# Performance work log

Hardware: AMD Instinct MI355X
Metric: run time of the kernel (lower is better)

The kernel has to match this reference:

```python
import jax, jax.numpy as jnp
import numpy as np

BATCH, EMBED, HIDDEN, VOCAB = 128, 512, 512, 32000
MAX_SEQ_LEN = 20  # self.max_seq_length in the torch module; static for jit


def setup_inputs() -> dict:
    key = jax.random.key(0)
    ks = jax.random.split(key, 9)
    w = lambda k, shape: (jax.random.normal(k, shape, jnp.float32) * 0.05)
    return {
        "features": jax.random.normal(ks[0], (BATCH, EMBED), jnp.float32),
        "lengths": jnp.full((BATCH,), MAX_SEQ_LEN, dtype=jnp.int32),
        "emb_table": w(ks[1], (VOCAB, EMBED)),
        # nn.LSTM (single layer) params, PyTorch gate order i,f,g,o
        "W_ih": w(ks[2], (4 * HIDDEN, EMBED)),
        "W_hh": w(ks[3], (4 * HIDDEN, HIDDEN)),
        "b_ih": w(ks[4], (4 * HIDDEN,)),
        "b_hh": w(ks[5], (4 * HIDDEN,)),
        # fc_out
        "W_fc": w(ks[6], (VOCAB, HIDDEN)),
        "b_fc": w(ks[7], (VOCAB,)),
    }


def reference(features, lengths, emb_table, W_ih, W_hh, b_ih, b_hh, W_fc, b_fc):
    B = features.shape[0]
    H = W_hh.shape[1]
    h0 = jnp.zeros((B, H), features.dtype)
    c0 = jnp.zeros((B, H), features.dtype)
    bias = b_ih + b_hh

    def step(carry, _):
        h, c, x = carry  # x: [B, E] current input token embedding
        gates = x @ W_ih.T + h @ W_hh.T + bias          # [B, 4H]
        i_g, f_g, g_g, o_g = jnp.split(gates, 4, axis=-1)
        c = jax.nn.sigmoid(f_g) * c + jax.nn.sigmoid(i_g) * jnp.tanh(g_g)
        h = jax.nn.sigmoid(o_g) * jnp.tanh(c)
        logits = h @ W_fc.T + b_fc                      # [B, V]
        idx = jnp.argmax(logits, axis=-1)               # greedy token
        val = jnp.max(logits, axis=-1)
        return (h, c, emb_table[idx]), (idx, val)

    _, (ids, vals) = jax.lax.scan(step, (h0, c0, features), None, length=MAX_SEQ_LEN)
    # [T, B] -> [B, T] to match torch.stack(..., 1)
    return jnp.transpose(ids), jnp.transpose(vals)
```

## Files before the change

kernel.cpp:

```cpp
#include <hip/hip_runtime.h>
#include <hip/hip_bf16.h>
#include <math.h>


#define B 128
#define E 512
#define H 512
#define V 32000
#define TSEQ 20
#define NG 2048
#define KSPLIT 16
#define NBLK_L 250
#define PKPAD 256

typedef __attribute__((ext_vector_type(8))) short short8v;
typedef __attribute__((ext_vector_type(4))) float f32x4;
typedef unsigned long long ull;

__device__ __forceinline__ float sigmoidf_(float x) { return 1.0f / (1.0f + expf(-x)); }

__device__ __forceinline__ short f2bf_s(float x) {
    __hip_bfloat16 h = __float2bfloat16(x);
    return *reinterpret_cast<short*>(&h);
}
__device__ __forceinline__ float bfs2f(short s) {
    __hip_bfloat16 h = *reinterpret_cast<__hip_bfloat16*>(&s);
    return __bfloat162float(h);
}
__device__ __forceinline__ ull shflx_u64(ull x, int m) {
    int lo = __shfl_xor((int)(unsigned int)x, m);
    int hi = __shfl_xor((int)(unsigned int)(x >> 32), m);
    return ((ull)(unsigned int)hi << 32) | (unsigned int)lo;
}
__device__ __forceinline__ void merge2(ull& k1, ull& k2, ull o1, ull o2) {
    ull a = k1 > o1 ? k1 : o1;
    ull b = k1 > o1 ? o1 : k1;
    ull c = k2 > o2 ? k2 : o2;
    k1 = a;
    k2 = b > c ? b : c;
}
__device__ __forceinline__ ull makekey(float v, unsigned int n) {
    unsigned int u = __float_as_uint(v);
    u ^= (unsigned int)(((int)u >> 31)) | 0x80000000u;
    return ((ull)u << 32) | (0xFFFFFFFFu - n);
}
__device__ __forceinline__ int keyidx(ull k) {
    return (int)(0xFFFFFFFFu - (unsigned int)(k & 0xFFFFFFFFu));
}

__global__ __launch_bounds__(256) void wsplit_pack_kernel(const float* __restrict__ W,
                                                          short* __restrict__ Wph,
                                                          short* __restrict__ Wpl) {
    size_t gid = (size_t)blockIdx.x * 256 + threadIdx.x;
    size_t i = gid * 8;
    int n = (int)(i >> 9);
    int k0 = (int)(i & 511);
    float4 a = *reinterpret_cast<const float4*>(W + i);
    float4 b = *reinterpret_cast<const float4*>(W + i + 4);
    float xv[8] = {a.x, a.y, a.z, a.w, b.x, b.y, b.z, b.w};
    union { short8v v; short s[8]; } uh, ul;
#pragma unroll
    for (int j = 0; j < 8; ++j) {
        short hs = f2bf_s(xv[j]);
        uh.s[j] = hs;
        ul.s[j] = f2bf_s(xv[j] - bfs2f(hs));
    }
    int nt = n >> 4, l15 = n & 15, cc = k0 >> 6, ks2 = (k0 >> 5) & 1, lg = (k0 >> 3) & 3;
    int lane = lg * 16 + l15;
    size_t off = ((((size_t)nt * 8 + cc) * 2 + ks2) * 64 + lane) * 8;
    *reinterpret_cast<short8v*>(Wph + off) = uh.v;
    *reinterpret_cast<short8v*>(Wpl + off) = ul.v;
}

__global__ __launch_bounds__(256) void init_kernel(const float* __restrict__ features,
                                                   float* __restrict__ xT,
                                                   float* __restrict__ hT,
                                                   float* __restrict__ cT) {
    int g = blockIdx.x * 256 + threadIdx.x;
    int j = g >> 7, b = g & 127;
    xT[g] = features[b * E + j];
    hT[g] = 0.0f;
    cT[g] = 0.0f;
}

__global__ __launch_bounds__(256) void gates_kernel(const float* __restrict__ xT,
                                                    const float* __restrict__ hT,
                                                    const float* __restrict__ W_ih,
                                                    const float* __restrict__ W_hh,
                                                    float* __restrict__ pT) {
    const int ntile = blockIdx.x;
    const int ks = blockIdx.y;
    const int tid = threadIdx.x;
    const int nt = tid & 15;
    const int bt = tid >> 4;
    __shared__ float xs[64][128];
    __shared__ float ws[128][64];
    const int kb = ks * 64;
    const bool isX = kb < E;
    const float* __restrict__ src = isX ? (xT + (size_t)kb * B) : (hT + (size_t)(kb - E) * B);
#pragma unroll
    for (int i = 0; i < 8; ++i) {
        int flat = i * 256 + tid;
        int kk = flat >> 5, b4 = flat & 31;
        *reinterpret_cast<float4*>(&xs[kk][b4 * 4]) =
            *reinterpret_cast<const float4*>(src + kk * B + b4 * 4);
    }
    {
        int r = tid >> 1, kh = tid & 1;
        int nglob = ntile * 128 + r;
        int jrow = nglob >> 2, g = nglob & 3;
        const float* __restrict__ Wp = isX ? (W_ih + (size_t)(g * H + jrow) * E + kb)
                                           : (W_hh + (size_t)(g * H + jrow) * H + (kb - E));
#pragma unroll
        for (int c = 0; c < 8; ++c) {
            int slot = (kh * 8 + c) ^ (r >> 3);
            *reinterpret_cast<float4*>(&ws[r][slot * 4]) =
                *reinterpret_cast<const float4*>(Wp + kh * 32 + c * 4);
        }
    }
    __syncthreads();
    float acc[8][8];
#pragma unroll
    for (int i = 0; i < 8; ++i)
#pragma unroll
        for (int j = 0; j < 8; ++j) acc[i][j] = 0.0f;

    for (int k4 = 0; k4 < 16; ++k4) {
        float wr[8][4];
#pragma unroll
        for (int ni = 0; ni < 8; ++ni) {
            int slot = k4 ^ nt;
            *reinterpret_cast<float4*>(wr[ni]) =
                *reinterpret_cast<const float4*>(&ws[nt * 8 + ni][slot * 4]);
        }
#pragma unroll
        for (int kk = 0; kk < 4; ++kk) {
            int k = k4 * 4 + kk;
            float4 x0 = *reinterpret_cast<const float4*>(&xs[k][bt * 8]);
            float4 x1 = *reinterpret_cast<const float4*>(&xs[k][bt * 8 + 4]);
            float xr[8] = {x0.x, x0.y, x0.z, x0.w, x1.x, x1.y, x1.z, x1.w};
#pragma unroll
            for (int bi = 0; bi < 8; ++bi)
#pragma unroll
                for (int ni = 0; ni < 8; ++ni) acc[bi][ni] += xr[bi] * wr[ni][kk];
        }
    }
#pragma unroll
    for (int ni = 0; ni < 8; ++ni) {
        size_t n = (size_t)ks * NG + ntile * 128 + nt * 8 + ni;
#pragma unroll
        for (int b4 = 0; b4 < 2; ++b4) {
            float4 col = make_float4(acc[b4 * 4 + 0][ni], acc[b4 * 4 + 1][ni],
                                     acc[b4 * 4 + 2][ni], acc[b4 * 4 + 3][ni]);
            *reinterpret_cast<float4*>(&pT[n * B + bt * 8 + b4 * 4]) = col;
        }
    }
}

__global__ __launch_bounds__(256) void cell_kernel(const float* __restrict__ pT,
                                                   const float* __restrict__ b_ih,
                                                   const float* __restrict__ b_hh,
                                                   float* __restrict__ cT,
                                                   float* __restrict__ hT,
                                                   short* __restrict__ h_hi,
                                                   short* __restrict__ h_lo,
                                                   float* __restrict__ h_bk) {
    int tid = threadIdx.x;
    int b = tid & 127;
    int j = blockIdx.x * 2 + (tid >> 7);
    float gs[4];
#pragma unroll
    for (int g = 0; g < 4; ++g) {
        float s = b_ih[g * H + j] + b_hh[g * H + j];
#pragma unroll
        for (int ks = 0; ks < KSPLIT; ++ks) s += pT[((size_t)ks * NG + 4 * j + g) * B + b];
        gs[g] = s;
    }
    float ig = sigmoidf_(gs[0]);
    float fg = sigmoidf_(gs[1]);
    float gg = tanhf(gs[2]);
    float og = sigmoidf_(gs[3]);
    float c = fg * cT[j * B + b] + ig * gg;
    cT[j * B + b] = c;
    float h = og * tanhf(c);
    hT[j * B + b] = h;
    h_bk[b * 512 + j] = h;
    short hs = f2bf_s(h);
    h_hi[b * 512 + j] = hs;
    h_lo[b * 512 + j] = f2bf_s(h - bfs2f(hs));
}

__global__ __launch_bounds__(512) void logits_kernel(const short* __restrict__ h_hi,
                                                     const short* __restrict__ h_lo,
                                                     const short* __restrict__ Wph,
                                                     const short* __restrict__ Wpl,
                                                     const float* __restrict__ b_fc,
                                                     ull* __restrict__ pk1,
                                                     ull* __restrict__ pk2) {
    const int bid = blockIdx.x;
    const int tid = threadIdx.x;
    const int w = tid >> 6;
    const int l = tid & 63;
    const int l15 = l & 15, lg = l >> 4;
    __shared__ union {
        short lh[2][128 * 64];
        struct { ull a1[4][128]; ull a2[4][128]; } ep;
    } sm;
    f32x4 acc[8][2];
#pragma unroll
    for (int mt = 0; mt < 8; ++mt)
#pragma unroll
        for (int ns = 0; ns < 2; ++ns) acc[mt][ns] = (f32x4){0.f, 0.f, 0.f, 0.f};

    short8v ph[2], pl[2];
    {
#pragma unroll
        for (int i = 0; i < 2; ++i) {
            int flat = tid + i * 512;
            int row = flat >> 3, c = flat & 7;
            ph[i] = *reinterpret_cast<const short8v*>(&h_hi[row * 512 + c * 8]);
            pl[i] = *reinterpret_cast<const short8v*>(&h_lo[row * 512 + c * 8]);
        }
    }
    for (int cc = 0; cc < 8; ++cc) {
        __syncthreads();
#pragma unroll
        for (int i = 0; i < 2; ++i) {
            int flat = tid + i * 512;
            int row = flat >> 3, c = flat & 7;
            int dst = row * 64 + ((c ^ (row & 7)) << 3);
            *reinterpret_cast<short8v*>(&sm.lh[0][dst]) = ph[i];
            *reinterpret_cast<short8v*>(&sm.lh[1][dst]) = pl[i];
        }
        __syncthreads();
        if (cc < 7) {
            const int kb = (cc + 1) * 64;
#pragma unroll
            for (int i = 0; i < 2; ++i) {
                int flat = tid + i * 512;
                int row = flat >> 3, c = flat & 7;
                ph[i] = *reinterpret_cast<const short8v*>(&h_hi[row * 512 + kb + c * 8]);
                pl[i] = *reinterpret_cast<const short8v*>(&h_lo[row * 512 + kb + c * 8]);
            }
        }
        if (w < 4) {
            short8v bh[2][2], bl[2][2];
#pragma unroll
            for (int ns = 0; ns < 2; ++ns) {
                int nt = bid * 8 + w * 2 + ns;
#pragma unroll
                for (int ks2 = 0; ks2 < 2; ++ks2) {
                    size_t off = ((((size_t)nt * 8 + cc) * 2 + ks2) * 64 + l) * 8;
                    bh[ns][ks2] = *reinterpret_cast<const short8v*>(&Wph[off]);
                    bl[ns][ks2] = *reinterpret_cast<const short8v*>(&Wpl[off]);
                }
            }
#pragma unroll
            for (int ks2 = 0; ks2 < 2; ++ks2) {
#pragma unroll
                for (int mt = 0; mt < 8; ++mt) {
                    int row = mt * 16 + l15;
                    int cslot = ks2 * 4 + lg;
                    int off = row * 64 + ((cslot ^ (row & 7)) << 3);
                    short8v ah = *reinterpret_cast<const short8v*>(&sm.lh[0][off]);
                    short8v al = *reinterpret_cast<const short8v*>(&sm.lh[1][off]);
#pragma unroll
                    for (int ns = 0; ns < 2; ++ns) {
                        acc[mt][ns] = __builtin_amdgcn_mfma_f32_16x16x32_bf16(ah, bh[ns][ks2], acc[mt][ns], 0, 0, 0);
                        acc[mt][ns] = __builtin_amdgcn_mfma_f32_16x16x32_bf16(ah, bl[ns][ks2], acc[mt][ns], 0, 0, 0);
                        acc[mt][ns] = __builtin_amdgcn_mfma_f32_16x16x32_bf16(al, bh[ns][ks2], acc[mt][ns], 0, 0, 0);
                    }
                }
            }
        }
    }
    __syncthreads();
    if (w < 4) {
        const int nr0 = bid * 128 + w * 32 + l15;
        const int nr1 = nr0 + 16;
        const float bias0 = b_fc[nr0];
        const float bias1 = b_fc[nr1];
#pragma unroll
        for (int mt = 0; mt < 8; ++mt) {
#pragma unroll
            for (int r = 0; r < 4; ++r) {
                ull k1 = makekey(acc[mt][0][r] + bias0, (unsigned)nr0);
                ull k2 = 0;
                merge2(k1, k2, makekey(acc[mt][1][r] + bias1, (unsigned)nr1), 0);
#pragma unroll
                for (int off = 1; off < 16; off <<= 1) {
                    ull o1 = shflx_u64(k1, off);
                    ull o2 = shflx_u64(k2, off);
                    merge2(k1, k2, o1, o2);
                }
                if (l15 == 0) {
                    int brow = mt * 16 + lg * 4 + r;
                    sm.ep.a1[w][brow] = k1;
                    sm.ep.a2[w][brow] = k2;
                }
            }
        }
    }
    __syncthreads();
    if (tid < 128) {
        ull k1 = sm.ep.a1[0][tid], k2 = sm.ep.a2[0][tid];
#pragma unroll
        for (int wv = 1; wv < 4; ++wv) merge2(k1, k2, sm.ep.a1[wv][tid], sm.ep.a2[wv][tid]);
        pk1[(size_t)tid * PKPAD + bid] = k1;
        pk2[(size_t)tid * PKPAD + bid] = k2;
    }
}

__global__ __launch_bounds__(256) void argmax_kernel(const ull* __restrict__ pk1,
                                                     const ull* __restrict__ pk2,
                                                     const float* __restrict__ h_bk,
                                                     const float* __restrict__ W_fc,
                                                     const float* __restrict__ b_fc,
                                                     const float* __restrict__ emb,
                                                     float* __restrict__ xT,
                                                     float* __restrict__ out,
                                                     int t) {
    const int b = blockIdx.x;
    const int tid = threadIdx.x;
    ull k1 = 0, k2 = 0;
    if (tid < NBLK_L) {
        k1 = pk1[(size_t)b * PKPAD + tid];
        k2 = pk2[(size_t)b * PKPAD + tid];
    }
#pragma unroll
    for (int off = 1; off < 64; off <<= 1)
        merge2(k1, k2, shflx_u64(k1, off), shflx_u64(k2, off));
    __shared__ ull sk1[4], sk2[4];
    __shared__ float part[4];
    __shared__ int s_i1, s_i2, s_w;
    if ((tid & 63) == 0) { sk1[tid >> 6] = k1; sk2[tid >> 6] = k2; }
    __syncthreads();
    if (tid == 0) {
        k1 = sk1[0]; k2 = sk2[0];
#pragma unroll
        for (int wv = 1; wv < 4; ++wv) merge2(k1, k2, sk1[wv], sk2[wv]);
        s_i1 = keyidx(k1);
        s_i2 = keyidx(k2);
    }
    __syncthreads();
    const int i1 = s_i1, i2 = s_i2;
    const int wv = tid >> 6, l = tid & 63;
    const int idx = (wv >> 1) ? i2 : i1;
    const int k0 = (wv & 1) * 256 + l * 4;
    float4 hv = *reinterpret_cast<const float4*>(&h_bk[(size_t)b * 512 + k0]);
    float4 wf = *reinterpret_cast<const float4*>(&W_fc[(size_t)idx * E + k0]);
    float hr[4] = {hv.x, hv.y, hv.z, hv.w};
    float wr[4] = {wf.x, wf.y, wf.z, wf.w};
    float s = 0.0f;
#pragma unroll
    for (int kk = 0; kk < 4; ++kk) s += hr[kk] * wr[kk];
#pragma unroll
    for (int off = 1; off < 64; off <<= 1) s += __shfl_xor(s, off);
    if (l == 0) part[wv] = s;
    __syncthreads();
    if (tid == 0) {
        float v0 = part[0] + part[1] + b_fc[i1];
        float v1 = part[2] + part[3] + b_fc[i2];
        int wi; float wvv;
        if (v1 > v0 || (v1 == v0 && i2 < i1)) { wi = i2; wvv = v1; }
        else { wi = i1; wvv = v0; }
        out[b * TSEQ + t] = (float)wi;
        out[B * TSEQ + b * TSEQ + t] = wvv;
        s_w = wi;
    }
    __syncthreads();
    const int widx = s_w;
    xT[(size_t)tid * B + b] = emb[(size_t)widx * E + tid];
    xT[(size_t)(tid + 256) * B + b] = emb[(size_t)widx * E + tid + 256];
}

extern "C" void kernel_launch(void* const* d_in, const int* in_sizes, int n_in,
                              void* d_out, int out_size, void* d_ws, size_t ws_size,
                              hipStream_t stream) {
    const float* features = (const float*)d_in[0];
    const float* emb  = (const float*)d_in[2];
    const float* W_ih = (const float*)d_in[3];
    const float* W_hh = (const float*)d_in[4];
    const float* b_ih = (const float*)d_in[5];
    const float* b_hh = (const float*)d_in[6];
    const float* W_fc = (const float*)d_in[7];
    const float* b_fc = (const float*)d_in[8];
    float* out = (float*)d_out;

    char* p = (char*)d_ws;
    short* Wph = (short*)p;       p += (size_t)V * E * 2;
    short* Wpl = (short*)p;       p += (size_t)V * E * 2;
    ull* pk1 = (ull*)p;           p += (size_t)B * PKPAD * 8;
    ull* pk2 = (ull*)p;           p += (size_t)B * PKPAD * 8;
    float* xT = (float*)p;        p += (size_t)E * B * 4;
    float* hT = (float*)p;        p += (size_t)E * B * 4;
    float* cT = (float*)p;        p += (size_t)E * B * 4;
    float* pT = (float*)p;        p += (size_t)KSPLIT * NG * B * 4;
    short* h_hi = (short*)p;      p += (size_t)E * B * 2;
    short* h_lo = (short*)p;      p += (size_t)E * B * 2;
    float* h_bk = (float*)p;      p += (size_t)E * B * 4;

    wsplit_pack_kernel<<<8000, 256, 0, stream>>>(W_fc, Wph, Wpl);
    init_kernel<<<256, 256, 0, stream>>>(features, xT, hT, cT);
    for (int t = 0; t < TSEQ; ++t) {
        gates_kernel<<<dim3(16, 16), 256, 0, stream>>>(xT, hT, W_ih, W_hh, pT);
        cell_kernel<<<256, 256, 0, stream>>>(pT, b_ih, b_hh, cT, hT, h_hi, h_lo, h_bk);
        logits_kernel<<<NBLK_L, 512, 0, stream>>>(h_hi, h_lo, Wph, Wpl, b_fc, pk1, pk2);
        argmax_kernel<<<B, 256, 0, stream>>>(pk1, pk2, h_bk, W_fc, b_fc, emb, xT, out, t);
    }
}
```

Before: 1.297 ms.

## Use single bf16 logits GEMM with top-4 candidate fp32 rescoring

Replaces the split hi/lo bf16 (3-MFMA) logits GEMM with a single plain bf16 MFMA pass, which removes the low-part weight and activation buffers and two thirds of the matrix ops. To keep argmax accuracy, the argmax kernel now merges a top-4 candidate list instead of top-2 and recomputes exact fp32 dot products for all four candidates before picking the winner. The pack kernel is also rewritten to iterate in output order, giving coalesced writes. The risk is that, with lower-precision scores, the true maximum may fall outside the top-4 candidates. Only two candidates per block are written to pk1/pk2, so slots 2-3 come only from merging across blocks.

```diff
diff --git a/kernel.cpp b/kernel.cpp
--- a/kernel.cpp
+++ b/kernel.cpp
@@ -23,10 +23,6 @@
     __hip_bfloat16 h = __float2bfloat16(x);
     return *reinterpret_cast<short*>(&h);
 }
-__device__ __forceinline__ float bfs2f(short s) {
-    __hip_bfloat16 h = *reinterpret_cast<__hip_bfloat16*>(&s);
-    return __bfloat162float(h);
-}
 __device__ __forceinline__ ull shflx_u64(ull x, int m) {
     int lo = __shfl_xor((int)(unsigned int)x, m);
     int hi = __shfl_xor((int)(unsigned int)(x >> 32), m);
@@ -39,6 +35,21 @@
     k1 = a;
     k2 = b > c ? b : c;
 }
+__device__ __forceinline__ void mergeQ(ull q[4], const ull o[4]) {
+    ull a0 = q[0], a1 = q[1], a2 = q[2], a3 = q[3];
+    ull b0 = o[0], b1 = o[1], b2 = o[2], b3 = o[3];
+    ull r[4];
+#pragma unroll
+    for (int i = 0; i < 4; ++i) {
+        bool t = a0 >= b0;
+        r[i] = t ? a0 : b0;
+        ull na0 = t ? a1 : a0, na1 = t ? a2 : a1, na2 = t ? a3 : a2, na3 = t ? 0ull : a3;
+        ull nb0 = t ? b0 : b1, nb1 = t ? b1 : b2, nb2 = t ? b2 : b3, nb3 = t ? b3 : 0ull;
+        a0 = na0; a1 = na1; a2 = na2; a3 = na3;
+        b0 = nb0; b1 = nb1; b2 = nb2; b3 = nb3;
+    }
+    q[0] = r[0]; q[1] = r[1]; q[2] = r[2]; q[3] = r[3];
+}
 __device__ __forceinline__ ull makekey(float v, unsigned int n) {
     unsigned int u = __float_as_uint(v);
     u ^= (unsigned int)(((int)u >> 31)) | 0x80000000u;
@@ -49,27 +60,20 @@
 }
 
 __global__ __launch_bounds__(256) void wsplit_pack_kernel(const float* __restrict__ W,
-                                                          short* __restrict__ Wph,
-                                                          short* __restrict__ Wpl) {
-    size_t gid = (size_t)blockIdx.x * 256 + threadIdx.x;
-    size_t i = gid * 8;
-    int n = (int)(i >> 9);
-    int k0 = (int)(i & 511);
-    float4 a = *reinterpret_cast<const float4*>(W + i);
-    float4 b = *reinterpret_cast<const float4*>(W + i + 4);
+                                                          short* __restrict__ Wph) {
+    unsigned s = blockIdx.x * 256 + threadIdx.x;
+    int lane = s & 63, l15 = lane & 15, lg = lane >> 4;
+    int ks2 = (s >> 6) & 1, cc = (s >> 7) & 7, nt = s >> 10;
+    int n = nt * 16 + l15;
+    int k = cc * 64 + ks2 * 32 + lg * 8;
+    const float* __restrict__ src = W + (size_t)n * E + k;
+    float4 a = *reinterpret_cast<const float4*>(src);
+    float4 b = *reinterpret_cast<const float4*>(src + 4);
     float xv[8] = {a.x, a.y, a.z, a.w, b.x, b.y, b.z, b.w};
-    union { short8v v; short s[8]; } uh, ul;
-#pragma unroll
-    for (int j = 0; j < 8; ++j) {
-        short hs = f2bf_s(xv[j]);
-        uh.s[j] = hs;
-        ul.s[j] = f2bf_s(xv[j] - bfs2f(hs));
-    }
-    int nt = n >> 4, l15 = n & 15, cc = k0 >> 6, ks2 = (k0 >> 5) & 1, lg = (k0 >> 3) & 3;
-    int lane = lg * 16 + l15;
-    size_t off = ((((size_t)nt * 8 + cc) * 2 + ks2) * 64 + lane) * 8;
-    *reinterpret_cast<short8v*>(Wph + off) = uh.v;
-    *reinterpret_cast<short8v*>(Wpl + off) = ul.v;
+    union { short8v v; short sh[8]; } uh;
+#pragma unroll
+    for (int j = 0; j < 8; ++j) uh.sh[j] = f2bf_s(xv[j]);
+    *reinterpret_cast<short8v*>(Wph + (size_t)s * 8) = uh.v;
 }
 
 __global__ __launch_bounds__(256) void init_kernel(const float* __restrict__ features,
@@ -163,7 +167,6 @@
                                                    float* __restrict__ cT,
                                                    float* __restrict__ hT,
                                                    short* __restrict__ h_hi,
-                                                   short* __restrict__ h_lo,
                                                    float* __restrict__ h_bk) {
     int tid = threadIdx.x;
     int b = tid & 127;
@@ -185,15 +188,11 @@
     float h = og * tanhf(c);
     hT[j * B + b] = h;
     h_bk[b * 512 + j] = h;
-    short hs = f2bf_s(h);
-    h_hi[b * 512 + j] = hs;
-    h_lo[b * 512 + j] = f2bf_s(h - bfs2f(hs));
+    h_hi[b * 512 + j] = f2bf_s(h);
 }
 
 __global__ __launch_bounds__(512) void logits_kernel(const short* __restrict__ h_hi,
-                                                     const short* __restrict__ h_lo,
                                                      const short* __restrict__ Wph,
-                                                     const short* __restrict__ Wpl,
                                                      const float* __restrict__ b_fc,
                                                      ull* __restrict__ pk1,
                                                      ull* __restrict__ pk2) {
@@ -203,7 +202,7 @@
     const int l = tid & 63;
     const int l15 = l & 15, lg = l >> 4;
     __shared__ union {
-        short lh[2][128 * 64];
+        short lh[128 * 64];
         struct { ull a1[4][128]; ull a2[4][128]; } ep;
     } sm;
     f32x4 acc[8][2];
@@ -212,15 +211,12 @@
 #pragma unroll
         for (int ns = 0; ns < 2; ++ns) acc[mt][ns] = (f32x4){0.f, 0.f, 0.f, 0.f};
 
-    short8v ph[2], pl[2];
-    {
-#pragma unroll
-        for (int i = 0; i < 2; ++i) {
-            int flat = tid + i * 512;
-            int row = flat >> 3, c = flat & 7;
-            ph[i] = *reinterpret_cast<const short8v*>(&h_hi[row * 512 + c * 8]);
-            pl[i] = *reinterpret_cast<const short8v*>(&h_lo[row * 512 + c * 8]);
-        }
+    short8v ph[2];
+#pragma unroll
+    for (int i = 0; i < 2; ++i) {
+        int flat = tid + i * 512;
+        int row = flat >> 3, c = flat & 7;
+        ph[i] = *reinterpret_cast<const short8v*>(&h_hi[row * 512 + c * 8]);
     }
     for (int cc = 0; cc < 8; ++cc) {
         __syncthreads();
@@ -229,8 +225,7 @@
             int flat = tid + i * 512;
             int row = flat >> 3, c = flat & 7;
             int dst = row * 64 + ((c ^ (row & 7)) << 3);
-            *reinterpret_cast<short8v*>(&sm.lh[0][dst]) = ph[i];
-            *reinterpret_cast<short8v*>(&sm.lh[1][dst]) = pl[i];
+            *reinterpret_cast<short8v*>(&sm.lh[dst]) = ph[i];
         }
         __syncthreads();
         if (cc < 7) {
@@ -240,11 +235,10 @@
                 int flat = tid + i * 512;
                 int row = flat >> 3, c = flat & 7;
                 ph[i] = *reinterpret_cast<const short8v*>(&h_hi[row * 512 + kb + c * 8]);
-                pl[i] = *reinterpret_cast<const short8v*>(&h_lo[row * 512 + kb + c * 8]);
             }
         }
         if (w < 4) {
-            short8v bh[2][2], bl[2][2];
+            short8v bh[2][2];
 #pragma unroll
             for (int ns = 0; ns < 2; ++ns) {
                 int nt = bid * 8 + w * 2 + ns;
@@ -252,7 +246,6 @@
                 for (int ks2 = 0; ks2 < 2; ++ks2) {
                     size_t off = ((((size_t)nt * 8 + cc) * 2 + ks2) * 64 + l) * 8;
                     bh[ns][ks2] = *reinterpret_cast<const short8v*>(&Wph[off]);
-                    bl[ns][ks2] = *reinterpret_cast<const short8v*>(&Wpl[off]);
                 }
             }
 #pragma unroll
@@ -262,14 +255,10 @@
                     int row = mt * 16 + l15;
                     int cslot = ks2 * 4 + lg;
                     int off = row * 64 + ((cslot ^ (row & 7)) << 3);
-                    short8v ah = *reinterpret_cast<const short8v*>(&sm.lh[0][off]);
-                    short8v al = *reinterpret_cast<const short8v*>(&sm.lh[1][off]);
-#pragma unroll
-                    for (int ns = 0; ns < 2; ++ns) {
+                    short8v ah = *reinterpret_cast<const short8v*>(&sm.lh[off]);
+#pragma unroll
+                    for (int ns = 0; ns < 2; ++ns)
                         acc[mt][ns] = __builtin_amdgcn_mfma_f32_16x16x32_bf16(ah, bh[ns][ks2], acc[mt][ns], 0, 0, 0);
-                        acc[mt][ns] = __builtin_amdgcn_mfma_f32_16x16x32_bf16(ah, bl[ns][ks2], acc[mt][ns], 0, 0, 0);
-                        acc[mt][ns] = __builtin_amdgcn_mfma_f32_16x16x32_bf16(al, bh[ns][ks2], acc[mt][ns], 0, 0, 0);
-                    }
                 }
             }
         }
@@ -322,48 +311,69 @@
                                                      int t) {
     const int b = blockIdx.x;
     const int tid = threadIdx.x;
-    ull k1 = 0, k2 = 0;
+    ull q[4] = {0, 0, 0, 0};
     if (tid < NBLK_L) {
-        k1 = pk1[(size_t)b * PKPAD + tid];
-        k2 = pk2[(size_t)b * PKPAD + tid];
-    }
-#pragma unroll
-    for (int off = 1; off < 64; off <<= 1)
-        merge2(k1, k2, shflx_u64(k1, off), shflx_u64(k2, off));
-    __shared__ ull sk1[4], sk2[4];
+        q[0] = pk1[(size_t)b * PKPAD + tid];
+        q[1] = pk2[(size_t)b * PKPAD + tid];
+    }
+#pragma unroll
+    for (int off = 1; off < 64; off <<= 1) {
+        ull oq[4];
+#pragma unroll
+        for (int j = 0; j < 4; ++j) oq[j] = shflx_u64(q[j], off);
+        mergeQ(q, oq);
+    }
+    __shared__ ull skq[4][4];
+    __shared__ float vex[4];
+    __shared__ int s_idx[4];
     __shared__ float part[4];
-    __shared__ int s_i1, s_i2, s_w;
-    if ((tid & 63) == 0) { sk1[tid >> 6] = k1; sk2[tid >> 6] = k2; }
+    __shared__ int s_w;
+    if ((tid & 63) == 0) {
+#pragma unroll
+        for (int j = 0; j < 4; ++j) skq[tid >> 6][j] = q[j];
+    }
     __syncthreads();
     if (tid == 0) {
-        k1 = sk1[0]; k2 = sk2[0];
-#pragma unroll
-        for (int wv = 1; wv < 4; ++wv) merge2(k1, k2, sk1[wv], sk2[wv]);
-        s_i1 = keyidx(k1);
-        s_i2 = keyidx(k2);
-    }
-    __syncthreads();
-    const int i1 = s_i1, i2 = s_i2;
+#pragma unroll
+        for (int j = 0; j < 4; ++j) q[j] = skq[0][j];
+#pragma unroll
+        for (int wv = 1; wv < 4; ++wv) mergeQ(q, skq[wv]);
+#pragma unroll
+        for (int j = 0; j < 4; ++j) s_idx[j] = keyidx(q[j]);
+    }
+    __syncthreads();
     const int wv = tid >> 6, l = tid & 63;
-    const int idx = (wv >> 1) ? i2 : i1;
-    const int k0 = (wv & 1) * 256 + l * 4;
-    float4 hv = *reinterpret_cast<const float4*>(&h_bk[(size_t)b * 512 + k0]);
-    float4 wf = *reinterpret_cast<const float4*>(&W_fc[(size_t)idx * E + k0]);
-    float hr[4] = {hv.x, hv.y, hv.z, hv.w};
-    float wr[4] = {wf.x, wf.y, wf.z, wf.w};
-    float s = 0.0f;
-#pragma unroll
-    for (int kk = 0; kk < 4; ++kk) s += hr[kk] * wr[kk];
-#pragma unroll
-    for (int off = 1; off < 64; off <<= 1) s += __shfl_xor(s, off);
-    if (l == 0) part[wv] = s;
-    __syncthreads();
+#pragma unroll
+    for (int pass = 0; pass < 2; ++pass) {
+        const int i1 = s_idx[pass * 2], i2 = s_idx[pass * 2 + 1];
+        const int idx = (wv >> 1) ? i2 : i1;
+        const int k0 = (wv & 1) * 256 + l * 4;
+        float4 hv = *reinterpret_cast<const float4*>(&h_bk[(size_t)b * 512 + k0]);
+        float4 wf = *reinterpret_cast<const float4*>(&W_fc[(size_t)idx * E + k0]);
+        float hr[4] = {hv.x, hv.y, hv.z, hv.w};
+        float wr[4] = {wf.x, wf.y, wf.z, wf.w};
+        float s = 0.0f;
+#pragma unroll
+        for (int kk = 0; kk < 4; ++kk) s += hr[kk] * wr[kk];
+#pragma unroll
+        for (int off = 1; off < 64; off <<= 1) s += __shfl_xor(s, off);
+        if (l == 0) part[wv] = s;
+        __syncthreads();
+        if (tid == 0) {
+            vex[pass * 2]     = part[0] + part[1] + b_fc[i1];
+            vex[pass * 2 + 1] = part[2] + part[3] + b_fc[i2];
+        }
+        __syncthreads();
+    }
     if (tid == 0) {
-        float v0 = part[0] + part[1] + b_fc[i1];
-        float v1 = part[2] + part[3] + b_fc[i2];
-        int wi; float wvv;
-        if (v1 > v0 || (v1 == v0 && i2 < i1)) { wi = i2; wvv = v1; }
-        else { wi = i1; wvv = v0; }
+        int wi = s_idx[0];
+        float wvv = vex[0];
+#pragma unroll
+        for (int c = 1; c < 4; ++c) {
+            float v = vex[c];
+            int ii = s_idx[c];
+            if (v > wvv || (v == wvv && ii < wi)) { wvv = v; wi = ii; }
+        }
         out[b * TSEQ + t] = (float)wi;
         out[B * TSEQ + b * TSEQ + t] = wvv;
         s_w = wi;
@@ -389,7 +399,6 @@
 
     char* p = (char*)d_ws;
     short* Wph = (short*)p;       p += (size_t)V * E * 2;
-    short* Wpl = (short*)p;       p += (size_t)V * E * 2;
     ull* pk1 = (ull*)p;           p += (size_t)B * PKPAD * 8;
     ull* pk2 = (ull*)p;           p += (size_t)B * PKPAD * 8;
     float* xT = (float*)p;        p += (size_t)E * B * 4;
@@ -397,15 +406,14 @@
     float* cT = (float*)p;        p += (size_t)E * B * 4;
     float* pT = (float*)p;        p += (size_t)KSPLIT * NG * B * 4;
     short* h_hi = (short*)p;      p += (size_t)E * B * 2;
-    short* h_lo = (short*)p;      p += (size_t)E * B * 2;
     float* h_bk = (float*)p;      p += (size_t)E * B * 4;
 
-    wsplit_pack_kernel<<<8000, 256, 0, stream>>>(W_fc, Wph, Wpl);
+    wsplit_pack_kernel<<<8000, 256, 0, stream>>>(W_fc, Wph);
     init_kernel<<<256, 256, 0, stream>>>(features, xT, hT, cT);
     for (int t = 0; t < TSEQ; ++t) {
         gates_kernel<<<dim3(16, 16), 256, 0, stream>>>(xT, hT, W_ih, W_hh, pT);
-        cell_kernel<<<256, 256, 0, stream>>>(pT, b_ih, b_hh, cT, hT, h_hi, h_lo, h_bk);
-        logits_kernel<<<NBLK_L, 512, 0, stream>>>(h_hi, h_lo, Wph, Wpl, b_fc, pk1, pk2);
+        cell_kernel<<<256, 256, 0, stream>>>(pT, b_ih, b_hh, cT, hT, h_hi, h_bk);
+        logits_kernel<<<NBLK_L, 512, 0, stream>>>(h_hi, Wph, b_fc, pk1, pk2);
         argmax_kernel<<<B, 256, 0, stream>>>(pk1, pk2, h_bk, W_fc, b_fc, emb, xT, out, t);
     }
 }
```

Result: faster. 1.169 ms (-9.9%).
